# Kernel tuning notes

Hardware: AMD Instinct MI355X
Metric: run time of the kernel (lower is better)

## Reference

```python
import jax, jax.numpy as jnp
import numpy as np

N_NODES = 50000
N_EDGES = 800000
IN_CH = 128
HID = 256
N_GRAPHS = 512


def setup_inputs() -> dict:
    key = jax.random.key(0)
    ks = jax.random.split(key, 10)
    x = jax.random.normal(ks[0], (N_NODES, IN_CH), dtype=jnp.float32)
    edge_index = jax.random.randint(ks[1], (2, N_EDGES), 0, N_NODES, dtype=jnp.int32)
    batch = jnp.sort(jax.random.randint(ks[2], (N_NODES,), 0, N_GRAPHS, dtype=jnp.int32))
    # GCNConv params (glorot-ish init)
    W0 = jax.random.normal(ks[3], (IN_CH, HID), dtype=jnp.float32) / np.sqrt(IN_CH)
    b0 = jnp.zeros((HID,), dtype=jnp.float32)
    W1 = jax.random.normal(ks[4], (HID, HID), dtype=jnp.float32) / np.sqrt(HID)
    b1 = jnp.zeros((HID,), dtype=jnp.float32)
    W2 = jax.random.normal(ks[5], (HID, HID), dtype=jnp.float32) / np.sqrt(HID)
    b2 = jnp.zeros((HID,), dtype=jnp.float32)
    return {"x": x, "W0": W0, "b0": b0, "W1": W1, "b1": b1, "W2": W2, "b2": b2,
            "edge_index": edge_index, "batch": batch}


def _gcn_norm(edge_index, num_nodes):
    # PyG gcn_norm with add_self_loops=True: A_hat = A + I, norm = D^-1/2 A_hat D^-1/2
    src, dst = edge_index[0], edge_index[1]
    loop = jnp.arange(num_nodes, dtype=src.dtype)
    src = jnp.concatenate([src, loop])
    dst = jnp.concatenate([dst, loop])
    deg = jax.ops.segment_sum(jnp.ones_like(dst, dtype=jnp.float32), dst,
                              num_segments=num_nodes)
    dinv = jnp.where(deg > 0, jax.lax.rsqrt(deg), 0.0)
    norm = dinv[src] * dinv[dst]  # [E + N]
    return src, dst, norm


def _gcn_conv(x, W, b, src, dst, norm, num_nodes):
    h = x @ W                                  # [N, out]
    msg = norm[:, None] * h[src]               # gather + scale, [E+N, out]
    out = jax.ops.segment_sum(msg, dst, num_segments=num_nodes)  # scatter-add
    return out + b


def reference(x, W0, b0, W1, b1, W2, b2, edge_index, batch):
    n = x.shape[0]
    src, dst, norm = _gcn_norm(edge_index, n)  # normalization is layer-independent
    h = jax.nn.relu(_gcn_conv(x, W0, b0, src, dst, norm, n))
    h = jax.nn.relu(_gcn_conv(h, W1, b1, src, dst, norm, n))
    h = jax.nn.relu(_gcn_conv(h, W2, b2, src, dst, norm, n))
    # global_add_pool: segment-sum node features by graph id
    return jax.ops.segment_sum(h, batch, num_segments=N_GRAPHS)
```

## Files before the change

kernel.cpp:

```cpp
#include <hip/hip_runtime.h>

constexpr int NN  = 50000;
constexpr int NE  = 800000;
constexpr int CIN = 128;
constexpr int CH  = 256;
constexpr int NG  = 512;

typedef unsigned short ushort_t;
typedef unsigned int uint_t;

static __device__ __forceinline__ ushort_t f2bf(float f) {
    uint_t u = __float_as_uint(f);
    u += 0x7fffu + ((u >> 16) & 1u);
    return (ushort_t)(u >> 16);
}

__global__ void conv_x_kernel(const float4* __restrict__ x, ushort4* __restrict__ xb, int n4) {
    int i = blockIdx.x * blockDim.x + threadIdx.x;
    if (i >= n4) return;
    float4 v = x[i];
    ushort4 o;
    o.x = f2bf(v.x); o.y = f2bf(v.y); o.z = f2bf(v.z); o.w = f2bf(v.w);
    xb[i] = o;
}

__global__ void conv_w_all_kernel(const float* __restrict__ W0, const float* __restrict__ W1,
                                  const float* __restrict__ W2, ushort_t* __restrict__ W0t,
                                  ushort_t* __restrict__ W1t, ushort_t* __restrict__ W2t) {
    int i = blockIdx.x * blockDim.x + threadIdx.x;
    if (i < CIN * CH) {
        int k = i / CH, n = i % CH;
        W0t[(size_t)n * CIN + k] = f2bf(W0[i]);
    } else if (i < CIN * CH + CH * CH) {
        int j = i - CIN * CH;
        int k = j / CH, n = j % CH;
        W1t[(size_t)n * CH + k] = f2bf(W1[j]);
    } else if (i < CIN * CH + 2 * CH * CH) {
        int j = i - CIN * CH - CH * CH;
        int k = j / CH, n = j % CH;
        W2t[(size_t)n * CH + k] = f2bf(W2[j]);
    }
}

__global__ void count_kernel(const int* __restrict__ dst, int* __restrict__ cnt, int E) {
    int e = blockIdx.x * blockDim.x + threadIdx.x;
    if (e < E) atomicAdd(&cnt[dst[e]], 1);
}

__global__ __launch_bounds__(256) void scan_bsum_kernel(const int* __restrict__ cnt,
                                                        int* __restrict__ bsum, int n) {
    int i = blockIdx.x * 256 + threadIdx.x;
    int v = (i < n) ? cnt[i] : 0;
    #pragma unroll
    for (int off = 32; off >= 1; off >>= 1) v += __shfl_xor(v, off, 64);
    __shared__ int ws[4];
    if ((threadIdx.x & 63) == 0) ws[threadIdx.x >> 6] = v;
    __syncthreads();
    if (threadIdx.x == 0) bsum[blockIdx.x] = ws[0] + ws[1] + ws[2] + ws[3];
}

__global__ __launch_bounds__(256) void scan_boff_kernel(int* __restrict__ bsum, int nb) {
    int tid = threadIdx.x, lane = tid & 63, wid = tid >> 6;
    int v = (tid < nb) ? bsum[tid] : 0;
    int s = v;
    #pragma unroll
    for (int off = 1; off < 64; off <<= 1) {
        int t = __shfl_up(s, off, 64);
        if (lane >= off) s += t;
    }
    __shared__ int wsum[4];
    if (lane == 63) wsum[wid] = s;
    __syncthreads();
    int wadd = 0;
    #pragma unroll
    for (int w = 0; w < 4; w++) if (w < wid) wadd += wsum[w];
    if (tid < nb) bsum[tid] = wadd + s - v;
}

__global__ __launch_bounds__(256) void scan_final_kernel(const int* __restrict__ cnt,
                                                         const int* __restrict__ boff,
                                                         int* __restrict__ rowptr,
                                                         float* __restrict__ dinv, int n) {
    int tid = threadIdx.x, lane = tid & 63, wid = tid >> 6;
    int i = blockIdx.x * 256 + tid;
    int v = (i < n) ? cnt[i] : 0;
    int s = v;
    #pragma unroll
    for (int off = 1; off < 64; off <<= 1) {
        int t = __shfl_up(s, off, 64);
        if (lane >= off) s += t;
    }
    __shared__ int wsum[4];
    if (lane == 63) wsum[wid] = s;
    __syncthreads();
    int wadd = boff[blockIdx.x];
    #pragma unroll
    for (int w = 0; w < 4; w++) if (w < wid) wadd += wsum[w];
    if (i < n) {
        rowptr[i] = wadd + s - v;
        dinv[i]   = rsqrtf((float)v + 1.0f);
        if (i == n - 1) rowptr[n] = wadd + s;
    }
}

__global__ void scatter_kernel(const int* __restrict__ src, const int* __restrict__ dst,
                               const int* __restrict__ rowptr, int* __restrict__ cursor,
                               const float* __restrict__ dinv, int2* __restrict__ epack, int E) {
    int e = blockIdx.x * blockDim.x + threadIdx.x;
    if (e >= E) return;
    int d = dst[e];
    int s = src[e];
    int p = rowptr[d] + atomicAdd(&cursor[d], 1);
    epack[p] = make_int2(s, __float_as_int(dinv[s]));
}

template <int C, int MODE>
__global__ __launch_bounds__(256) void node_agg_kernel(
    const ushort_t* __restrict__ h, const int* __restrict__ rowptr,
    const int2* __restrict__ epack, const float* __restrict__ dinv,
    const float* __restrict__ bias, const int* __restrict__ batch,
    void* __restrict__ out_v, int n) {
    constexpr int V = C / 64;
    constexpr int UF = 16;
    int wave = threadIdx.x >> 6;
    int lane = threadIdx.x & 63;
    int d = blockIdx.x * 4 + wave;
    if (d >= n) return;

    int beg = rowptr[d], end = rowptr[d + 1];
    float acc[V] = {};

    for (int e = beg; e < end; e += UF) {
        int   srcs[UF];
        float wts[UF];
        #pragma unroll
        for (int u = 0; u < UF; u++) {
            int idx = e + u;
            int2 ep = epack[min(idx, NE - 1)];
            bool a = idx < end;
            srcs[u] = a ? ep.x : d;
            wts[u]  = a ? __int_as_float(ep.y) : 0.0f;
        }
        if constexpr (V == 4) {
            uint_t ra[UF], rb[UF];
            #pragma unroll
            for (int u = 0; u < UF; u++) {
                const uint_t* row = (const uint_t*)(h + (size_t)srcs[u] * C);
                ra[u] = row[lane];
                rb[u] = row[64 + lane];
            }
            #pragma unroll
            for (int u = 0; u < UF; u++) {
                float w = wts[u];
                acc[0] += w * __uint_as_float(ra[u] << 16);
                acc[1] += w * __uint_as_float(ra[u] & 0xffff0000u);
                acc[2] += w * __uint_as_float(rb[u] << 16);
                acc[3] += w * __uint_as_float(rb[u] & 0xffff0000u);
            }
        } else {
            uint_t rv[UF];
            #pragma unroll
            for (int u = 0; u < UF; u++)
                rv[u] = ((const uint_t*)(h + (size_t)srcs[u] * C))[lane];
            #pragma unroll
            for (int u = 0; u < UF; u++) {
                float w = wts[u];
                acc[0] += w * __uint_as_float(rv[u] << 16);
                acc[1] += w * __uint_as_float(rv[u] & 0xffff0000u);
            }
        }
    }

    float dd = dinv[d];
    float self[V];
    {
        const uint_t* row = (const uint_t*)(h + (size_t)d * C);
        uint_t sa = row[lane];
        self[0] = __uint_as_float(sa << 16);
        self[1] = __uint_as_float(sa & 0xffff0000u);
        if constexpr (V == 4) {
            uint_t sb = row[64 + lane];
            self[2] = __uint_as_float(sb << 16);
            self[3] = __uint_as_float(sb & 0xffff0000u);
        }
    }

    float r[V];
    if constexpr (MODE >= 1) {
        float2 bA = *(const float2*)(bias + 2 * lane);
        r[0] = fmaxf(dd * acc[0] + dd * dd * self[0] + bA.x, 0.0f);
        r[1] = fmaxf(dd * acc[1] + dd * dd * self[1] + bA.y, 0.0f);
        if constexpr (V == 4) {
            float2 bB = *(const float2*)(bias + 128 + 2 * lane);
            r[2] = fmaxf(dd * acc[2] + dd * dd * self[2] + bB.x, 0.0f);
            r[3] = fmaxf(dd * acc[3] + dd * dd * self[3] + bB.y, 0.0f);
        }
    } else {
        #pragma unroll
        for (int i = 0; i < V; i++)
            r[i] = dd * acc[i] + dd * dd * self[i];
    }

    if constexpr (MODE == 2) {
        float* o = (float*)out_v + (size_t)batch[d] * C;
        atomicAdd(o + 2 * lane, r[0]);
        atomicAdd(o + 2 * lane + 1, r[1]);
        if constexpr (V == 4) {
            atomicAdd(o + 128 + 2 * lane, r[2]);
            atomicAdd(o + 128 + 2 * lane + 1, r[3]);
        }
    } else {
        uint_t* o = (uint_t*)((ushort_t*)out_v + (size_t)d * C);
        o[lane] = (uint_t)f2bf(r[0]) | ((uint_t)f2bf(r[1]) << 16);
        if constexpr (V == 4)
            o[64 + lane] = (uint_t)f2bf(r[2]) | ((uint_t)f2bf(r[3]) << 16);
    }
}

typedef __attribute__((ext_vector_type(8))) short bf16x8;
typedef __attribute__((ext_vector_type(4))) float f32x4;

template <int MODE>
__global__ __launch_bounds__(256) void gemm_bf16_kernel(
    const ushort_t* __restrict__ A, const ushort_t* __restrict__ Wt,
    const float* __restrict__ bias, ushort_t* __restrict__ C, int M, int K) {
    __shared__ ushort_t As[128][40];
    __shared__ ushort_t Bs[128][40];
    int tid = threadIdx.x;
    int row0 = blockIdx.x * 128, col0 = blockIdx.y * 128;
    int lr = tid >> 2, lq = tid & 3;
    int lane = tid & 63, wv = tid >> 6;
    int wr = (wv >> 1) * 64, wc = (wv & 1) * 64;
    int r16 = lane & 15, quad = lane >> 4;

    int gr0 = row0 + lr, gr1 = row0 + lr + 64;
    const ushort_t* pa0 = A + (size_t)gr0 * K + lq * 8;
    const ushort_t* pa1 = A + (size_t)gr1 * K + lq * 8;
    const ushort_t* pb0 = Wt + (size_t)(col0 + lr) * K + lq * 8;
    const ushort_t* pb1 = Wt + (size_t)(col0 + lr + 64) * K + lq * 8;
    bool va0 = gr0 < M, va1 = gr1 < M;

    f32x4 acc[4][4] = {};

    uint4 a0 = make_uint4(0, 0, 0, 0), a1 = make_uint4(0, 0, 0, 0);
    if (va0) a0 = *(const uint4*)pa0;
    if (va1) a1 = *(const uint4*)pa1;
    uint4 b0 = *(const uint4*)pb0;
    uint4 b1 = *(const uint4*)pb1;

    for (int k0 = 0; k0 < K; k0 += 32) {
        *(uint4*)&As[lr][lq * 8]      = a0;
        *(uint4*)&As[lr + 64][lq * 8] = a1;
        *(uint4*)&Bs[lr][lq * 8]      = b0;
        *(uint4*)&Bs[lr + 64][lq * 8] = b1;
        __syncthreads();

        int kn = k0 + 32;
        if (kn < K) {
            a0 = va0 ? *(const uint4*)(pa0 + kn) : make_uint4(0, 0, 0, 0);
            a1 = va1 ? *(const uint4*)(pa1 + kn) : make_uint4(0, 0, 0, 0);
            b0 = *(const uint4*)(pb0 + kn);
            b1 = *(const uint4*)(pb1 + kn);
        }

        bf16x8 af[4], bfr[4];
        #pragma unroll
        for (int i = 0; i < 4; i++) af[i]  = *(const bf16x8*)&As[wr + i * 16 + r16][quad * 8];
        #pragma unroll
        for (int j = 0; j < 4; j++) bfr[j] = *(const bf16x8*)&Bs[wc + j * 16 + r16][quad * 8];
        #pragma unroll
        for (int i = 0; i < 4; i++)
            #pragma unroll
            for (int j = 0; j < 4; j++)
                acc[i][j] = __builtin_amdgcn_mfma_f32_16x16x32_bf16(af[i], bfr[j], acc[i][j], 0, 0, 0);
        __syncthreads();
    }

    #pragma unroll
    for (int j = 0; j < 4; j++) {
        int colc = col0 + wc + j * 16 + r16;
        float bval = (MODE == 1) ? bias[colc] : 0.0f;
        #pragma unroll
        for (int i = 0; i < 4; i++) {
            #pragma unroll
            for (int r = 0; r < 4; r++) {
                int row = row0 + wr + i * 16 + quad * 4 + r;
                if (row < M) {
                    float v = acc[i][j][r];
                    if (MODE == 1) v = fmaxf(v + bval, 0.0f);
                    C[(size_t)row * 256 + colc] = f2bf(v);
                }
            }
        }
    }
}

extern "C" void kernel_launch(void* const* d_in, const int* in_sizes, int n_in,
                              void* d_out, int out_size, void* d_ws, size_t ws_size,
                              hipStream_t stream) {
    const float* x   = (const float*)d_in[0];
    const float* W0  = (const float*)d_in[1];
    const float* b0  = (const float*)d_in[2];
    const float* W1  = (const float*)d_in[3];
    const float* b1  = (const float*)d_in[4];
    const float* W2  = (const float*)d_in[5];
    const float* b2  = (const float*)d_in[6];
    const int*   ei  = (const int*)d_in[7];
    const int*   src = ei;
    const int*   dst = ei + NE;
    const int*   batch = (const int*)d_in[8];
    float* out = (float*)d_out;

    char* ws = (char*)d_ws;
    ushort_t* Abf = (ushort_t*)ws;
    ushort_t* Bbf = (ushort_t*)(ws + 25600000ull);
    ushort_t* xbf = (ushort_t*)(ws + 51200000ull);
    ushort_t* W0t = (ushort_t*)(ws + 64000000ull);
    ushort_t* W1t = (ushort_t*)(ws + 64065536ull);
    ushort_t* W2t = (ushort_t*)(ws + 64196608ull);
    float*    dinv   = (float*)(ws + 64327680ull);
    int*      rowptr = (int*)  (ws + 64527680ull);
    int*      cnt    = (int*)  (ws + 64727808ull);
    int2*     epack  = (int2*) (ws + 64927808ull);
    int*      bsum   = (int*)  (ws + 71327808ull);

    const int scanBlocks = (NN + 255) / 256;
    const int nodeBlocks = (NN + 3) / 4;
    const dim3 ggrid((NN + 127) / 128, 2);
    const int wElems = CIN * CH + 2 * CH * CH;

    conv_x_kernel<<<(NN * CIN / 4 + 255) / 256, 256, 0, stream>>>((const float4*)x, (ushort4*)xbf, NN * CIN / 4);
    conv_w_all_kernel<<<(wElems + 255) / 256, 256, 0, stream>>>(W0, W1, W2, W0t, W1t, W2t);

    hipMemsetAsync(cnt, 0, (size_t)NN * 4, stream);
    count_kernel<<<(NE + 255) / 256, 256, 0, stream>>>(dst, cnt, NE);
    scan_bsum_kernel<<<scanBlocks, 256, 0, stream>>>(cnt, bsum, NN);
    scan_boff_kernel<<<1, 256, 0, stream>>>(bsum, scanBlocks);
    scan_final_kernel<<<scanBlocks, 256, 0, stream>>>(cnt, bsum, rowptr, dinv, NN);
    hipMemsetAsync(cnt, 0, (size_t)NN * 4, stream);
    scatter_kernel<<<(NE + 255) / 256, 256, 0, stream>>>(src, dst, rowptr, cnt, dinv, epack, NE);

    node_agg_kernel<CIN, 0><<<nodeBlocks, 256, 0, stream>>>(xbf, rowptr, epack, dinv, nullptr, nullptr, Bbf, NN);
    gemm_bf16_kernel<1><<<ggrid, 256, 0, stream>>>(Bbf, W0t, b0, Abf, NN, CIN);

    gemm_bf16_kernel<0><<<ggrid, 256, 0, stream>>>(Abf, W1t, nullptr, Bbf, NN, CH);
    node_agg_kernel<CH, 1><<<nodeBlocks, 256, 0, stream>>>(Bbf, rowptr, epack, dinv, b1, nullptr, Abf, NN);

    gemm_bf16_kernel<0><<<ggrid, 256, 0, stream>>>(Abf, W2t, nullptr, Bbf, NN, CH);
    hipMemsetAsync(out, 0, (size_t)NG * CH * 4, stream);
    node_agg_kernel<CH, 2><<<nodeBlocks, 256, 0, stream>>>(Bbf, rowptr, epack, dinv, b2, batch, out, NN);
}
```

Before: 468.8 us.

## Fold self-loops into CSR and aggregate by feature slices across blocks

After: 772.5 us. +64.8%, slower.

```diff
diff --git a/kernel.cpp b/kernel.cpp
--- a/kernel.cpp
+++ b/kernel.cpp
@@ -2,6 +2,7 @@
 
 constexpr int NN  = 50000;
 constexpr int NE  = 800000;
+constexpr int NEA = NE + NN;
 constexpr int CIN = 128;
 constexpr int CH  = 256;
 constexpr int NG  = 512;
@@ -14,6 +15,8 @@
     u += 0x7fffu + ((u >> 16) & 1u);
     return (ushort_t)(u >> 16);
 }
+static __device__ __forceinline__ float blo(uint_t v) { return __uint_as_float(v << 16); }
+static __device__ __forceinline__ float bhi(uint_t v) { return __uint_as_float(v & 0xffff0000u); }
 
 __global__ void conv_x_kernel(const float4* __restrict__ x, ushort4* __restrict__ xb, int n4) {
     int i = blockIdx.x * blockDim.x + threadIdx.x;
@@ -42,6 +45,11 @@
     }
 }
 
+__global__ void set_one_kernel(int* __restrict__ cnt, int n) {
+    int i = blockIdx.x * blockDim.x + threadIdx.x;
+    if (i < n) cnt[i] = 1;
+}
+
 __global__ void count_kernel(const int* __restrict__ dst, int* __restrict__ cnt, int E) {
     int e = blockIdx.x * blockDim.x + threadIdx.x;
     if (e < E) atomicAdd(&cnt[dst[e]], 1);
@@ -98,122 +106,88 @@
     for (int w = 0; w < 4; w++) if (w < wid) wadd += wsum[w];
     if (i < n) {
         rowptr[i] = wadd + s - v;
-        dinv[i]   = rsqrtf((float)v + 1.0f);
+        dinv[i]   = rsqrtf((float)v);
         if (i == n - 1) rowptr[n] = wadd + s;
     }
 }
 
-__global__ void scatter_kernel(const int* __restrict__ src, const int* __restrict__ dst,
-                               const int* __restrict__ rowptr, int* __restrict__ cursor,
-                               const float* __restrict__ dinv, int2* __restrict__ epack, int E) {
+__global__ void scatter_self_kernel(const int* __restrict__ src, const int* __restrict__ dst,
+                                    const int* __restrict__ rowptr, int* __restrict__ cursor,
+                                    const float* __restrict__ dinv, int2* __restrict__ epack,
+                                    int E, int n) {
     int e = blockIdx.x * blockDim.x + threadIdx.x;
-    if (e >= E) return;
-    int d = dst[e];
-    int s = src[e];
-    int p = rowptr[d] + atomicAdd(&cursor[d], 1);
-    epack[p] = make_int2(s, __float_as_int(dinv[s]));
+    if (e < E) {
+        int d = dst[e], s = src[e];
+        int p = rowptr[d] + atomicAdd(&cursor[d], 1);
+        epack[p] = make_int2(s, __float_as_int(dinv[s]));
+    } else if (e < E + n) {
+        int i = e - E;
+        epack[rowptr[i + 1] - 1] = make_int2(i, __float_as_int(dinv[i]));
+    }
 }
 
 template <int C, int MODE>
-__global__ __launch_bounds__(256) void node_agg_kernel(
+__global__ __launch_bounds__(256) void slice_agg_kernel(
     const ushort_t* __restrict__ h, const int* __restrict__ rowptr,
     const int2* __restrict__ epack, const float* __restrict__ dinv,
     const float* __restrict__ bias, const int* __restrict__ batch,
     void* __restrict__ out_v, int n) {
-    constexpr int V = C / 64;
-    constexpr int UF = 16;
-    int wave = threadIdx.x >> 6;
-    int lane = threadIdx.x & 63;
-    int d = blockIdx.x * 4 + wave;
-    if (d >= n) return;
-
-    int beg = rowptr[d], end = rowptr[d + 1];
-    float acc[V] = {};
-
-    for (int e = beg; e < end; e += UF) {
-        int   srcs[UF];
-        float wts[UF];
-        #pragma unroll
-        for (int u = 0; u < UF; u++) {
-            int idx = e + u;
-            int2 ep = epack[min(idx, NE - 1)];
-            bool a = idx < end;
-            srcs[u] = a ? ep.x : d;
-            wts[u]  = a ? __int_as_float(ep.y) : 0.0f;
-        }
-        if constexpr (V == 4) {
-            uint_t ra[UF], rb[UF];
-            #pragma unroll
-            for (int u = 0; u < UF; u++) {
-                const uint_t* row = (const uint_t*)(h + (size_t)srcs[u] * C);
-                ra[u] = row[lane];
-                rb[u] = row[64 + lane];
+    constexpr int CPS = C / 8;
+    constexpr int LPG = CPS / 2;
+    int s = blockIdx.x & 7;
+    int chunk = blockIdx.x >> 3;
+    int wave = threadIdx.x >> 6, lane = threadIdx.x & 63;
+    int g = lane / LPG, sl = lane % LPG;
+    int d0 = chunk * 64 + wave * 16;
+    const ushort_t* hs = h + s * CPS;
+
+    for (int di = 0; di < 16; di++) {
+        int d = d0 + di;
+        if (d >= n) break;
+        int beg = rowptr[d], end = rowptr[d + 1];
+        float a0 = 0.f, a1 = 0.f;
+        for (int eb = beg; eb < end; eb += 8) {
+            if constexpr (C == 256) {
+                int i0 = eb + g * 2, i1 = i0 + 1;
+                int2 e0 = epack[min(i0, NEA - 1)];
+                int2 e1 = epack[min(i1, NEA - 1)];
+                float w0 = (i0 < end) ? __int_as_float(e0.y) : 0.f;
+                float w1 = (i1 < end) ? __int_as_float(e1.y) : 0.f;
+                uint_t f0 = *(const uint_t*)(hs + (size_t)e0.x * C + sl * 2);
+                uint_t f1 = *(const uint_t*)(hs + (size_t)e1.x * C + sl * 2);
+                a0 += w0 * blo(f0) + w1 * blo(f1);
+                a1 += w0 * bhi(f0) + w1 * bhi(f1);
+            } else {
+                int i0 = eb + g;
+                int2 e0 = epack[min(i0, NEA - 1)];
+                float w0 = (i0 < end) ? __int_as_float(e0.y) : 0.f;
+                uint_t f0 = *(const uint_t*)(hs + (size_t)e0.x * C + sl * 2);
+                a0 += w0 * blo(f0);
+                a1 += w0 * bhi(f0);
             }
-            #pragma unroll
-            for (int u = 0; u < UF; u++) {
-                float w = wts[u];
-                acc[0] += w * __uint_as_float(ra[u] << 16);
-                acc[1] += w * __uint_as_float(ra[u] & 0xffff0000u);
-                acc[2] += w * __uint_as_float(rb[u] << 16);
-                acc[3] += w * __uint_as_float(rb[u] & 0xffff0000u);
+        }
+        #pragma unroll
+        for (int off = LPG; off < 64; off <<= 1) {
+            a0 += __shfl_xor(a0, off, 64);
+            a1 += __shfl_xor(a1, off, 64);
+        }
+        float dd = dinv[d];
+        float v0 = dd * a0, v1 = dd * a1;
+        if constexpr (MODE >= 1) {
+            int c0 = s * CPS + sl * 2;
+            v0 = fmaxf(v0 + bias[c0], 0.f);
+            v1 = fmaxf(v1 + bias[c0 + 1], 0.f);
+        }
+        if (g == 0) {
+            if constexpr (MODE == 2) {
+                float* o = (float*)out_v + (size_t)batch[d] * C + s * CPS + sl * 2;
+                atomicAdd(o, v0);
+                atomicAdd(o + 1, v1);
+            } else {
+                uint_t pv = (uint_t)f2bf(v0) | ((uint_t)f2bf(v1) << 16);
+                *(uint_t*)((ushort_t*)out_v + (size_t)d * C + s * CPS + sl * 2) = pv;
             }
-        } else {
-            uint_t rv[UF];
-            #pragma unroll
-            for (int u = 0; u < UF; u++)
-                rv[u] = ((const uint_t*)(h + (size_t)srcs[u] * C))[lane];
-            #pragma unroll
-            for (int u = 0; u < UF; u++) {
-                float w = wts[u];
-                acc[0] += w * __uint_as_float(rv[u] << 16);
-                acc[1] += w * __uint_as_float(rv[u] & 0xffff0000u);
-            }
-        }
-    }
-
-    float dd = dinv[d];
-    float self[V];
-    {
-        const uint_t* row = (const uint_t*)(h + (size_t)d * C);
-        uint_t sa = row[lane];
-        self[0] = __uint_as_float(sa << 16);
-        self[1] = __uint_as_float(sa & 0xffff0000u);
-        if constexpr (V == 4) {
-            uint_t sb = row[64 + lane];
-            self[2] = __uint_as_float(sb << 16);
-            self[3] = __uint_as_float(sb & 0xffff0000u);
-        }
-    }
-
-    float r[V];
-    if constexpr (MODE >= 1) {
-        float2 bA = *(const float2*)(bias + 2 * lane);
-        r[0] = fmaxf(dd * acc[0] + dd * dd * self[0] + bA.x, 0.0f);
-        r[1] = fmaxf(dd * acc[1] + dd * dd * self[1] + bA.y, 0.0f);
-        if constexpr (V == 4) {
-            float2 bB = *(const float2*)(bias + 128 + 2 * lane);
-            r[2] = fmaxf(dd * acc[2] + dd * dd * self[2] + bB.x, 0.0f);
-            r[3] = fmaxf(dd * acc[3] + dd * dd * self[3] + bB.y, 0.0f);
-        }
-    } else {
-        #pragma unroll
-        for (int i = 0; i < V; i++)
-            r[i] = dd * acc[i] + dd * dd * self[i];
-    }
-
-    if constexpr (MODE == 2) {
-        float* o = (float*)out_v + (size_t)batch[d] * C;
-        atomicAdd(o + 2 * lane, r[0]);
-        atomicAdd(o + 2 * lane + 1, r[1]);
-        if constexpr (V == 4) {
-            atomicAdd(o + 128 + 2 * lane, r[2]);
-            atomicAdd(o + 128 + 2 * lane + 1, r[3]);
-        }
-    } else {
-        uint_t* o = (uint_t*)((ushort_t*)out_v + (size_t)d * C);
-        o[lane] = (uint_t)f2bf(r[0]) | ((uint_t)f2bf(r[1]) << 16);
-        if constexpr (V == 4)
-            o[64 + lane] = (uint_t)f2bf(r[2]) | ((uint_t)f2bf(r[3]) << 16);
+        }
     }
 }
 
@@ -322,31 +296,31 @@
     int*      rowptr = (int*)  (ws + 64527680ull);
     int*      cnt    = (int*)  (ws + 64727808ull);
     int2*     epack  = (int2*) (ws + 64927808ull);
-    int*      bsum   = (int*)  (ws + 71327808ull);
+    int*      bsum   = (int*)  (ws + 71727808ull);
 
     const int scanBlocks = (NN + 255) / 256;
-    const int nodeBlocks = (NN + 3) / 4;
+    const int sliceBlocks = 8 * ((NN + 63) / 64);
     const dim3 ggrid((NN + 127) / 128, 2);
     const int wElems = CIN * CH + 2 * CH * CH;
 
     conv_x_kernel<<<(NN * CIN / 4 + 255) / 256, 256, 0, stream>>>((const float4*)x, (ushort4*)xbf, NN * CIN / 4);
     conv_w_all_kernel<<<(wElems + 255) / 256, 256, 0, stream>>>(W0, W1, W2, W0t, W1t, W2t);
 
-    hipMemsetAsync(cnt, 0, (size_t)NN * 4, stream);
+    set_one_kernel<<<scanBlocks, 256, 0, stream>>>(cnt, NN);
     count_kernel<<<(NE + 255) / 256, 256, 0, stream>>>(dst, cnt, NE);
     scan_bsum_kernel<<<scanBlocks, 256, 0, stream>>>(cnt, bsum, NN);
     scan_boff_kernel<<<1, 256, 0, stream>>>(bsum, scanBlocks);
     scan_final_kernel<<<scanBlocks, 256, 0, stream>>>(cnt, bsum, rowptr, dinv, NN);
     hipMemsetAsync(cnt, 0, (size_t)NN * 4, stream);
-    scatter_kernel<<<(NE + 255) / 256, 256, 0, stream>>>(src, dst, rowptr, cnt, dinv, epack, NE);
-
-    node_agg_kernel<CIN, 0><<<nodeBlocks, 256, 0, stream>>>(xbf, rowptr, epack, dinv, nullptr, nullptr, Bbf, NN);
+    scatter_self_kernel<<<(NEA + 255) / 256, 256, 0, stream>>>(src, dst, rowptr, cnt, dinv, epack, NE, NN);
+
+    slice_agg_kernel<CIN, 0><<<sliceBlocks, 256, 0, stream>>>(xbf, rowptr, epack, dinv, nullptr, nullptr, Bbf, NN);
     gemm_bf16_kernel<1><<<ggrid, 256, 0, stream>>>(Bbf, W0t, b0, Abf, NN, CIN);
 
     gemm_bf16_kernel<0><<<ggrid, 256, 0, stream>>>(Abf, W1t, nullptr, Bbf, NN, CH);
-    node_agg_kernel<CH, 1><<<nodeBlocks, 256, 0, stream>>>(Bbf, rowptr, epack, dinv, b1, nullptr, Abf, NN);
+    slice_agg_kernel<CH, 1><<<sliceBlocks, 256, 0, stream>>>(Bbf, rowptr, epack, dinv, b1, nullptr, Abf, NN);
 
     gemm_bf16_kernel<0><<<ggrid, 256, 0, stream>>>(Abf, W2t, nullptr, Bbf, NN, CH);
     hipMemsetAsync(out, 0, (size_t)NG * CH * 4, stream);
-    node_agg_kernel<CH, 2><<<nodeBlocks, 256, 0, stream>>>(Bbf, rowptr, epack, dinv, b2, batch, out, NN);
-}
+    slice_agg_kernel<CH, 2><<<sliceBlocks, 256, 0, stream>>>(Bbf, rowptr, epack, dinv, b2, batch, out, NN);
+}
```

## Fold self-loops into CSR and split aggregation by XCD-local column slices

Applied to the files above, without the earlier changes.

Result: slower. 1.032 ms (+120.2%).

```diff
diff --git a/kernel.cpp b/kernel.cpp
--- a/kernel.cpp
+++ b/kernel.cpp
@@ -2,6 +2,7 @@
 
 constexpr int NN  = 50000;
 constexpr int NE  = 800000;
+constexpr int NEA = NE + NN;
 constexpr int CIN = 128;
 constexpr int CH  = 256;
 constexpr int NG  = 512;
@@ -14,6 +15,8 @@
     u += 0x7fffu + ((u >> 16) & 1u);
     return (ushort_t)(u >> 16);
 }
+static __device__ __forceinline__ float blo(uint_t v) { return __uint_as_float(v << 16); }
+static __device__ __forceinline__ float bhi(uint_t v) { return __uint_as_float(v & 0xffff0000u); }
 
 __global__ void conv_x_kernel(const float4* __restrict__ x, ushort4* __restrict__ xb, int n4) {
     int i = blockIdx.x * blockDim.x + threadIdx.x;
@@ -42,6 +45,11 @@
     }
 }
 
+__global__ void set_one_kernel(int* __restrict__ cnt, int n) {
+    int i = blockIdx.x * blockDim.x + threadIdx.x;
+    if (i < n) cnt[i] = 1;
+}
+
 __global__ void count_kernel(const int* __restrict__ dst, int* __restrict__ cnt, int E) {
     int e = blockIdx.x * blockDim.x + threadIdx.x;
     if (e < E) atomicAdd(&cnt[dst[e]], 1);
@@ -98,20 +106,24 @@
     for (int w = 0; w < 4; w++) if (w < wid) wadd += wsum[w];
     if (i < n) {
         rowptr[i] = wadd + s - v;
-        dinv[i]   = rsqrtf((float)v + 1.0f);
+        dinv[i]   = rsqrtf((float)v);
         if (i == n - 1) rowptr[n] = wadd + s;
     }
 }
 
-__global__ void scatter_kernel(const int* __restrict__ src, const int* __restrict__ dst,
-                               const int* __restrict__ rowptr, int* __restrict__ cursor,
-                               const float* __restrict__ dinv, int2* __restrict__ epack, int E) {
+__global__ void scatter_self_kernel(const int* __restrict__ src, const int* __restrict__ dst,
+                                    const int* __restrict__ rowptr, int* __restrict__ cursor,
+                                    const float* __restrict__ dinv, int2* __restrict__ epack,
+                                    int E, int n) {
     int e = blockIdx.x * blockDim.x + threadIdx.x;
-    if (e >= E) return;
-    int d = dst[e];
-    int s = src[e];
-    int p = rowptr[d] + atomicAdd(&cursor[d], 1);
-    epack[p] = make_int2(s, __float_as_int(dinv[s]));
+    if (e < E) {
+        int d = dst[e], s = src[e];
+        int p = rowptr[d] + atomicAdd(&cursor[d], 1);
+        epack[p] = make_int2(s, __float_as_int(dinv[s]));
+    } else if (e < E + n) {
+        int i = e - E;
+        epack[rowptr[i + 1] - 1] = make_int2(i, __float_as_int(dinv[i]));
+    }
 }
 
 template <int C, int MODE>
@@ -121,7 +133,7 @@
     const float* __restrict__ bias, const int* __restrict__ batch,
     void* __restrict__ out_v, int n) {
     constexpr int V = C / 64;
-    constexpr int UF = 16;
+    constexpr int UF = 8;
     int wave = threadIdx.x >> 6;
     int lane = threadIdx.x & 63;
     int d = blockIdx.x * 4 + wave;
@@ -136,7 +148,7 @@
         #pragma unroll
         for (int u = 0; u < UF; u++) {
             int idx = e + u;
-            int2 ep = epack[min(idx, NE - 1)];
+            int2 ep = epack[min(idx, NEA - 1)];
             bool a = idx < end;
             srcs[u] = a ? ep.x : d;
             wts[u]  = a ? __int_as_float(ep.y) : 0.0f;
@@ -152,10 +164,10 @@
             #pragma unroll
             for (int u = 0; u < UF; u++) {
                 float w = wts[u];
-                acc[0] += w * __uint_as_float(ra[u] << 16);
-                acc[1] += w * __uint_as_float(ra[u] & 0xffff0000u);
-                acc[2] += w * __uint_as_float(rb[u] << 16);
-                acc[3] += w * __uint_as_float(rb[u] & 0xffff0000u);
+                acc[0] += w * blo(ra[u]);
+                acc[1] += w * bhi(ra[u]);
+                acc[2] += w * blo(rb[u]);
+                acc[3] += w * bhi(rb[u]);
             }
         } else {
             uint_t rv[UF];
@@ -165,40 +177,26 @@
             #pragma unroll
             for (int u = 0; u < UF; u++) {
                 float w = wts[u];
-                acc[0] += w * __uint_as_float(rv[u] << 16);
-                acc[1] += w * __uint_as_float(rv[u] & 0xffff0000u);
+                acc[0] += w * blo(rv[u]);
+                acc[1] += w * bhi(rv[u]);
             }
         }
     }
 
     float dd = dinv[d];
-    float self[V];
-    {
-        const uint_t* row = (const uint_t*)(h + (size_t)d * C);
-        uint_t sa = row[lane];
-        self[0] = __uint_as_float(sa << 16);
-        self[1] = __uint_as_float(sa & 0xffff0000u);
-        if constexpr (V == 4) {
-            uint_t sb = row[64 + lane];
-            self[2] = __uint_as_float(sb << 16);
-            self[3] = __uint_as_float(sb & 0xffff0000u);
-        }
-    }
-
     float r[V];
     if constexpr (MODE >= 1) {
         float2 bA = *(const float2*)(bias + 2 * lane);
-        r[0] = fmaxf(dd * acc[0] + dd * dd * self[0] + bA.x, 0.0f);
-        r[1] = fmaxf(dd * acc[1] + dd * dd * self[1] + bA.y, 0.0f);
+        r[0] = fmaxf(dd * acc[0] + bA.x, 0.0f);
+        r[1] = fmaxf(dd * acc[1] + bA.y, 0.0f);
         if constexpr (V == 4) {
             float2 bB = *(const float2*)(bias + 128 + 2 * lane);
-            r[2] = fmaxf(dd * acc[2] + dd * dd * self[2] + bB.x, 0.0f);
-            r[3] = fmaxf(dd * acc[3] + dd * dd * self[3] + bB.y, 0.0f);
+            r[2] = fmaxf(dd * acc[2] + bB.x, 0.0f);
+            r[3] = fmaxf(dd * acc[3] + bB.y, 0.0f);
         }
     } else {
         #pragma unroll
-        for (int i = 0; i < V; i++)
-            r[i] = dd * acc[i] + dd * dd * self[i];
+        for (int i = 0; i < V; i++) r[i] = dd * acc[i];
     }
 
     if constexpr (MODE == 2) {
@@ -214,6 +212,68 @@
         o[lane] = (uint_t)f2bf(r[0]) | ((uint_t)f2bf(r[1]) << 16);
         if constexpr (V == 4)
             o[64 + lane] = (uint_t)f2bf(r[2]) | ((uint_t)f2bf(r[3]) << 16);
+    }
+}
+
+template <int MODE>
+__global__ __launch_bounds__(256) void xcd_agg_kernel(
+    const ushort_t* __restrict__ h, const int* __restrict__ rowptr,
+    const int2* __restrict__ epack, const float* __restrict__ dinv,
+    const float* __restrict__ bias, const int* __restrict__ batch,
+    void* __restrict__ out_v, int* __restrict__ wctr, int n) {
+    constexpr int C = 256;
+    __shared__ int sh_chunk;
+    const int nChunks = (n + 63) / 64;
+    uint_t xcd;
+    asm volatile("s_getreg_b32 %0, hwreg(HW_REG_XCC_ID)" : "=s"(xcd));
+    xcd &= 7;
+    int wave = threadIdx.x >> 6, lane = threadIdx.x & 63;
+    int g = lane >> 4, sl = lane & 15;
+
+    for (int si = 0; si < 8; si++) {
+        int s = (xcd + si) & 7;
+        const ushort_t* hs = h + s * 32;
+        while (true) {
+            __syncthreads();
+            if (threadIdx.x == 0) sh_chunk = atomicAdd(&wctr[s], 1);
+            __syncthreads();
+            int chunk = sh_chunk;
+            if (chunk >= nChunks) break;
+            int d0 = chunk * 64 + wave * 16;
+            for (int di = 0; di < 16; di++) {
+                int d = d0 + di;
+                if (d >= n) break;
+                int beg = rowptr[d], end = rowptr[d + 1];
+                float a0 = 0.f, a1 = 0.f;
+                for (int eb = beg; eb < end; eb += 8) {
+                    int i0 = eb + g * 2, i1 = i0 + 1;
+                    int2 e0 = epack[min(i0, NEA - 1)];
+                    int2 e1 = epack[min(i1, NEA - 1)];
+                    float w0 = (i0 < end) ? __int_as_float(e0.y) : 0.f;
+                    float w1 = (i1 < end) ? __int_as_float(e1.y) : 0.f;
+                    uint_t f0 = *(const uint_t*)(hs + (size_t)e0.x * C + sl * 2);
+                    uint_t f1 = *(const uint_t*)(hs + (size_t)e1.x * C + sl * 2);
+                    a0 += w0 * blo(f0) + w1 * blo(f1);
+                    a1 += w0 * bhi(f0) + w1 * bhi(f1);
+                }
+                a0 += __shfl_xor(a0, 16, 64); a1 += __shfl_xor(a1, 16, 64);
+                a0 += __shfl_xor(a0, 32, 64); a1 += __shfl_xor(a1, 32, 64);
+                float dd = dinv[d];
+                int c0 = s * 32 + sl * 2;
+                float v0 = fmaxf(dd * a0 + bias[c0], 0.f);
+                float v1 = fmaxf(dd * a1 + bias[c0 + 1], 0.f);
+                if (g == 0) {
+                    if constexpr (MODE == 2) {
+                        float* o = (float*)out_v + (size_t)batch[d] * C + c0;
+                        atomicAdd(o, v0);
+                        atomicAdd(o + 1, v1);
+                    } else {
+                        uint_t pv = (uint_t)f2bf(v0) | ((uint_t)f2bf(v1) << 16);
+                        *(uint_t*)((ushort_t*)out_v + (size_t)d * C + c0) = pv;
+                    }
+                }
+            }
+        }
     }
 }
 
@@ -322,31 +382,33 @@
     int*      rowptr = (int*)  (ws + 64527680ull);
     int*      cnt    = (int*)  (ws + 64727808ull);
     int2*     epack  = (int2*) (ws + 64927808ull);
-    int*      bsum   = (int*)  (ws + 71327808ull);
+    int*      bsum   = (int*)  (ws + 71727808ull);
+    int*      wctr   = (int*)  (ws + 71728832ull);
 
     const int scanBlocks = (NN + 255) / 256;
     const int nodeBlocks = (NN + 3) / 4;
     const dim3 ggrid((NN + 127) / 128, 2);
     const int wElems = CIN * CH + 2 * CH * CH;
 
+    hipMemsetAsync(wctr, 0, 64, stream);
     conv_x_kernel<<<(NN * CIN / 4 + 255) / 256, 256, 0, stream>>>((const float4*)x, (ushort4*)xbf, NN * CIN / 4);
     conv_w_all_kernel<<<(wElems + 255) / 256, 256, 0, stream>>>(W0, W1, W2, W0t, W1t, W2t);
 
-    hipMemsetAsync(cnt, 0, (size_t)NN * 4, stream);
+    set_one_kernel<<<scanBlocks, 256, 0, stream>>>(cnt, NN);
     count_kernel<<<(NE + 255) / 256, 256, 0, stream>>>(dst, cnt, NE);
     scan_bsum_kernel<<<scanBlocks, 256, 0, stream>>>(cnt, bsum, NN);
     scan_boff_kernel<<<1, 256, 0, stream>>>(bsum, scanBlocks);
     scan_final_kernel<<<scanBlocks, 256, 0, stream>>>(cnt, bsum, rowptr, dinv, NN);
     hipMemsetAsync(cnt, 0, (size_t)NN * 4, stream);
-    scatter_kernel<<<(NE + 255) / 256, 256, 0, stream>>>(src, dst, rowptr, cnt, dinv, epack, NE);
+    scatter_self_kernel<<<(NEA + 255) / 256, 256, 0, stream>>>(src, dst, rowptr, cnt, dinv, epack, NE, NN);
 
     node_agg_kernel<CIN, 0><<<nodeBlocks, 256, 0, stream>>>(xbf, rowptr, epack, dinv, nullptr, nullptr, Bbf, NN);
     gemm_bf16_kernel<1><<<ggrid, 256, 0, stream>>>(Bbf, W0t, b0, Abf, NN, CIN);
 
     gemm_bf16_kernel<0><<<ggrid, 256, 0, stream>>>(Abf, W1t, nullptr, Bbf, NN, CH);
-    node_agg_kernel<CH, 1><<<nodeBlocks, 256, 0, stream>>>(Bbf, rowptr, epack, dinv, b1, nullptr, Abf, NN);
+    xcd_agg_kernel<1><<<2048, 256, 0, stream>>>(Bbf, rowptr, epack, dinv, b1, nullptr, Abf, wctr, NN);
 
     gemm_bf16_kernel<0><<<ggrid, 256, 0, stream>>>(Abf, W2t, nullptr, Bbf, NN, CH);
     hipMemsetAsync(out, 0, (size_t)NG * CH * 4, stream);
-    node_agg_kernel<CH, 2><<<nodeBlocks, 256, 0, stream>>>(Bbf, rowptr, epack, dinv, b2, batch, out, NN);
-}
+    xcd_agg_kernel<2><<<2048, 256, 0, stream>>>(Bbf, rowptr, epack, dinv, b2, batch, out, wctr + 8, NN);
+}
```
